# Kernel optimization log

Hardware: AMD Instinct MI355X
Metric: run time of the kernel (lower is better)

The kernel has to match this reference:

```python
import jax, jax.numpy as jnp
import numpy as np

N = 4096          # number of points in the minibatch
POINT_DIM = 64    # latent/data dimensionality used to synthesize valid distance matrices


def _pairwise_dist(x):
    # x: [N, D] -> [N, N] Euclidean distance matrix
    sq = jnp.sum(x * x, axis=1)
    d2 = sq[:, None] + sq[None, :] - 2.0 * (x @ x.T)
    d = jnp.sqrt(jnp.maximum(d2, 0.0))
    return d * (1.0 - jnp.eye(x.shape[0], dtype=x.dtype))  # exact zero diagonal


def _mst_pairs(D):
    """0-dim Vietoris-Rips persistence pairs == edges of the minimum spanning tree.

    Vectorized Prim's algorithm: lax.scan over N-1 steps, O(N) per step.
    Returns int32 [N-1, 2] (parent, child) edge index pairs. Indices are
    non-differentiable (matches the .detach() in the original module).
    """
    D = jax.lax.stop_gradient(D)
    n = D.shape[0]
    INF = jnp.asarray(jnp.inf, D.dtype)
    in_tree = jnp.zeros(n, dtype=bool).at[0].set(True)
    min_dist = D[0].at[0].set(INF)          # best known edge weight from tree to each node
    parent = jnp.zeros(n, dtype=jnp.int32)  # tree endpoint realizing that edge

    def step(carry, _):
        min_dist, parent, in_tree = carry
        masked = jnp.where(in_tree, INF, min_dist)
        j = jnp.argmin(masked).astype(jnp.int32)
        pair = jnp.stack([parent[j], j])
        in_tree = in_tree.at[j].set(True)
        better = (D[j] < min_dist) & (~in_tree)
        parent = jnp.where(better, j, parent)
        min_dist = jnp.where(better, D[j], min_dist)
        return (min_dist, parent, in_tree), pair

    _, pairs = jax.lax.scan(step, (min_dist, parent, in_tree), None, length=n - 1)
    return pairs  # [N-1, 2]


def _sig_error(s1, s2):
    # ((s1 - s2) ** 2).sum() ** 0.5
    diff = s1 - s2
    return jnp.sqrt(jnp.sum(diff * diff))


def _gather(D, pairs):
    return D[pairs[:, 0], pairs[:, 1]]


def setup_inputs() -> dict:
    key = jax.random.key(0)
    k1, k2 = jax.random.split(key)
    x1 = jax.random.normal(k1, (N, POINT_DIM), dtype=jnp.float32)
    x2 = jax.random.normal(k2, (N, POINT_DIM), dtype=jnp.float32)
    return {
        "distances1": _pairwise_dist(x1),
        "distances2": _pairwise_dist(x2),
    }


def reference(distances1, distances2):
    # pairs: 0-dim persistence pairings (MST edges), computed on detached distances
    pairs1 = _mst_pairs(distances1)
    pairs2 = _mst_pairs(distances2)

    # match_edges == 'symmetric'
    sig1 = _gather(distances1, pairs1)
    sig1_2 = _gather(distances2, pairs1)
    sig2 = _gather(distances2, pairs2)
    sig2_1 = _gather(distances1, pairs2)

    distance1_2 = _sig_error(sig1, sig1_2)
    distance2_1 = _sig_error(sig2, sig2_1)
    distance = distance1_2 + distance2_1

    # metrics.matched_pairs: |set(pairs1) ∩ set(pairs2)| (MST edges are unique)
    eq = (pairs1[:, None, :] == pairs2[None, :, :]).all(-1)  # [N-1, N-1]
    matched_pairs = jnp.sum(eq.any(-1)).astype(jnp.float32)

    return distance, distance1_2, distance2_1, matched_pairs
```

## Files before the change

### kernel.cpp

```cpp
#include <hip/hip_runtime.h>
#include <math.h>

#define N 4096
#define ROUNDS 12
#define INFKEY 0xFFFFFFFFFFFFFFFFULL
#define LCAP 48
#define EC (N - 1)
#define M2 (2 * EC)
#define MBLK 32
#define RPB (N / MBLK)
#define RPW (RPB / 16)

typedef unsigned long long u64;
typedef unsigned int u32;
typedef unsigned short u16;

#define WS_PARENT(ws) ((int*)((char*)(ws) + 0))
#define WS_RCNT(ws)   ((int*)((char*)(ws) + 32768))
#define WS_RTHR(ws)   ((float*)((char*)(ws) + 65536))
#define WS_EDGES(ws)  ((int2*)((char*)(ws) + 98304))
#define WS_CAND(ws)   ((u64*)((char*)(ws) + 163840))
#define WS_META(ws)   ((int*)((char*)(ws) + 294912))
#define WS_LISTS(ws)  ((u64*)((char*)(ws) + 295168))


__device__ __forceinline__ void mat_barrier(int* cnt, int* gen, int target) {
    __syncthreads();
    if (threadIdx.x == 0) {
        __threadfence();
        int old = atomicAdd(cnt, 1);
        if (old == MBLK - 1) {
            __hip_atomic_store(cnt, 0, __ATOMIC_RELAXED, __HIP_MEMORY_SCOPE_AGENT);
            __hip_atomic_store(gen, target, __ATOMIC_RELEASE, __HIP_MEMORY_SCOPE_AGENT);
        } else {
            while (__hip_atomic_load(gen, __ATOMIC_ACQUIRE, __HIP_MEMORY_SCOPE_AGENT) < target)
                __builtin_amdgcn_s_sleep(1);
        }
        __threadfence();
    }
    __syncthreads();
}

__global__ __launch_bounds__(1024) void build_kernel(const float* __restrict__ D1,
                                                     const float* __restrict__ D2,
                                                     int* __restrict__ rowcount,
                                                     float* __restrict__ rthresh,
                                                     u64* __restrict__ lists,
                                                     u64* __restrict__ cand,
                                                     int* __restrict__ meta) {
    const int gb = blockIdx.x;
    const int tid = threadIdx.x;

    if (gb < 4) {
        int i = (gb * 1024 + tid) * 4;
        cand[i] = INFKEY; cand[i + 1] = INFKEY; cand[i + 2] = INFKEY; cand[i + 3] = INFKEY;
    } else if (gb == 4 && tid < 64) {
        meta[tid] = 0;
    }

    const int m = gb >> 8;
    const int wid = tid >> 6, lane = tid & 63;
    const int row = (gb & 255) * 16 + wid;
    const float* __restrict__ Drow = (m ? D2 : D1) + (size_t)row * N;
    const float INF = __builtin_inff();

    float4 v[16];
#pragma unroll
    for (int it = 0; it < 16; ++it)
        v[it] = *(const float4*)(Drow + it * 256 + lane * 4);

    float mn = INF, sm = 0.f;
#pragma unroll
    for (int it = 0; it < 16; ++it) {
        float a = v[it].x, b = v[it].y, c = v[it].z, d = v[it].w;
        mn = fminf(mn, a > 0.f ? a : INF);
        mn = fminf(mn, b > 0.f ? b : INF);
        mn = fminf(mn, c > 0.f ? c : INF);
        mn = fminf(mn, d > 0.f ? d : INF);
        sm += a + b + c + d;
    }
#pragma unroll
    for (int off = 32; off > 0; off >>= 1) {
        mn = fminf(mn, __shfl_xor(mn, off, 64));
        sm += __shfl_xor(sm, off, 64);
    }
    const float mean = sm * (1.f / 4095.f);
    float T = mn + 0.25f * (mean - mn);

    int mycnt, total;
    for (int iter = 0; iter < 10; ++iter) {
        mycnt = 0;
#pragma unroll
        for (int it = 0; it < 16; ++it) {
            mycnt += (v[it].x > 0.f && v[it].x < T);
            mycnt += (v[it].y > 0.f && v[it].y < T);
            mycnt += (v[it].z > 0.f && v[it].z < T);
            mycnt += (v[it].w > 0.f && v[it].w < T);
        }
        total = mycnt;
#pragma unroll
        for (int off = 32; off > 0; off >>= 1) total += __shfl_xor(total, off, 64);
        if (total <= LCAP) break;
        T = mn + 0.5f * (T - mn);
    }

    int incl = mycnt;
#pragma unroll
    for (int d = 1; d < 64; d <<= 1) {
        int o = __shfl_up(incl, d, 64);
        if (lane >= d) incl += o;
    }
    int pos = incl - mycnt;

    u64* lp = lists + ((size_t)m * N + row) * LCAP;
#pragma unroll
    for (int it = 0; it < 16; ++it) {
        float e4[4] = {v[it].x, v[it].y, v[it].z, v[it].w};
#pragma unroll
        for (int s = 0; s < 4; ++s) {
            float x = e4[s];
            if (x > 0.f && x < T) {
                if (pos < LCAP)
                    lp[pos] = ((u64)__float_as_uint(x) << 12) | (unsigned)(it * 256 + lane * 4 + s);
                ++pos;
            }
        }
    }
    if (lane == 0) {
        rowcount[m * N + row] = total;
        rthresh[m * N + row] = T;
    }
}

__global__ __launch_bounds__(1024) void solve_kernel(const float* __restrict__ D1,
                                                     const float* __restrict__ D2,
                                                     const int* __restrict__ rcnt,
                                                     const float* __restrict__ rthr,
                                                     const u64* __restrict__ lists,
                                                     u64* __restrict__ cand_g,
                                                     int2* __restrict__ edges_g,
                                                     int* __restrict__ parent_g,
                                                     int* __restrict__ meta,
                                                     float* __restrict__ out) {
    const int b = blockIdx.x;
    const int m = b / MBLK;
    const int bm = b - m * MBLK;
    const int tid = threadIdx.x;
    const int wid = tid >> 6, lane = tid & 63;
    const float* __restrict__ D = m ? D2 : D1;
    const int* __restrict__ grc = rcnt + m * N;
    const float* __restrict__ gth = rthr + m * N;
    const u64* __restrict__ gls = lists + (size_t)m * N * LCAP;
    int2* __restrict__ ged = edges_g + (size_t)m * N;
    int* __restrict__ gpar = parent_g + m * N;
    int* bcnt = meta + m * 16 + 1;
    int* bgen = meta + m * 16 + 2;
    int* garr = meta + 40;
    const float INF = __builtin_inff();

    __shared__ __align__(16) char SM[57344];
    int* scomp = (int*)SM;
    u64* scand = (u64*)(SM + 16384);
    u16* sresc = (u16*)(SM + 49152);
    __shared__ int snres, secnt, scnt, swar[16];

    for (int i = tid; i < N; i += 1024) scomp[i] = i;
    if (tid == 0) secnt = 0;
    int phase = 0;
    bool done = false;

    for (int round = 0; round < ROUNDS && !done; ++round) {
        const int buf = round & 1;
        u64* __restrict__ gcand = cand_g + (size_t)buf * 2 * N + m * N;
        u64* __restrict__ gcand_o = cand_g + (size_t)(buf ^ 1) * 2 * N + m * N;

        for (int i = tid; i < N; i += 1024) scand[i] = INFKEY;
        if (tid == 0) snres = 0;
        __syncthreads();

        for (int r = 0; r < RPW; ++r) {
            const int row = bm * RPB + wid * RPW + r;
            const int c = scomp[row];
            const int cnt = grc[row];
            const bool forced = (cnt > LCAP);
            u64 best = INFKEY;
            if (!forced && lane < cnt) {
                u64 e = gls[(size_t)row * LCAP + lane];
                int j = (int)(e & 0xFFF);
                if (scomp[j] != c) best = e;
            }
#pragma unroll
            for (int off = 32; off > 0; off >>= 1) {
                u64 o = __shfl_xor(best, off, 64);
                if (o < best) best = o;
            }
            if (lane == 0) {
                if (best != INFKEY) {
                    u64 key = ((best >> 12) << 24) | ((u64)row << 12) | (best & 0xFFF);
                    if (key < scand[c]) atomicMin(&scand[c], key);
                } else {
                    int i = atomicAdd(&snres, 1);
                    sresc[i] = (u16)(row | (forced ? 0x4000 : 0x1000));
                }
            }
        }
        __syncthreads();
        for (int c = tid; c < N; c += 1024) {
            u64 v = scand[c];
            if (v != INFKEY) atomicMin(&gcand[c], v);
        }
        mat_barrier(bcnt, bgen, ++phase);

        for (int i = tid + bm * 0; i < RPB; i += 1024)
            if (tid < RPB) gcand_o[bm * RPB + tid] = INFKEY;
        for (int i = tid; i < snres; i += 1024) {
            u16 e = sresc[i];
            if (e & 0x1000) {
                int row = e & 0xFFF;
                int c = scomp[row];
                u64 cc = gcand[c];
                float w = (cc == INFKEY) ? INF : __uint_as_float((u32)(cc >> 24));
                if (!(gth[row] < w)) sresc[i] = 0xFFFF;
            }
        }
        __syncthreads();
        {
            const int nres = snres;
            for (int i = wid; i < nres; i += 16) {
                u16 e = sresc[i];
                if (e == 0xFFFF) continue;
                int row = (int)(e & 0xFFF);
                int c = scomp[row];
                const float* Drow = D + (size_t)row * N;
                u64 best = INFKEY;
                for (int j0 = lane * 4; j0 < N; j0 += 256) {
                    float4 d = *(const float4*)(Drow + j0);
                    int4 cj = *(const int4*)(scomp + j0);
                    if (cj.x != c) { u64 k = ((u64)__float_as_uint(d.x) << 12) | (unsigned)(j0 + 0); if (k < best) best = k; }
                    if (cj.y != c) { u64 k = ((u64)__float_as_uint(d.y) << 12) | (unsigned)(j0 + 1); if (k < best) best = k; }
                    if (cj.z != c) { u64 k = ((u64)__float_as_uint(d.z) << 12) | (unsigned)(j0 + 2); if (k < best) best = k; }
                    if (cj.w != c) { u64 k = ((u64)__float_as_uint(d.w) << 12) | (unsigned)(j0 + 3); if (k < best) best = k; }
                }
#pragma unroll
                for (int off = 32; off > 0; off >>= 1) {
                    u64 o = __shfl_xor(best, off, 64);
                    if (o < best) best = o;
                }
                if (lane == 0 && best != INFKEY) {
                    u64 key = ((best >> 12) << 24) | ((u64)row << 12) | (best & 0xFFF);
                    atomicMin(&gcand[c], key);
                }
            }
        }
        mat_barrier(bcnt, bgen, ++phase);

        for (int i = tid; i < N; i += 1024) scand[i] = gcand[i];
        __syncthreads();
        u16* slink = sresc;
        for (int c = tid; c < N; c += 1024) {
            int l = scomp[c];
            if (l == c) {
                u64 k = scand[c];
                if (k != INFKEY) {
                    int v = (int)(k & 0xFFF);
                    int u = (int)((k >> 12) & 0xFFF);
                    int t = scomp[v];
                    u64 tk = scand[t];
                    int mutual = 0;
                    if (tk != INFKEY) {
                        int tv = (int)(tk & 0xFFF);
                        mutual = (scomp[tv] == c);
                    }
                    if (mutual) {
                        if (c < t) {
                            if (bm == 0) { int idx = atomicAdd(&secnt, 1); ged[idx] = make_int2(u, v); }
                        } else l = t;
                    } else {
                        if (bm == 0) { int idx = atomicAdd(&secnt, 1); ged[idx] = make_int2(u, v); }
                        l = t;
                    }
                }
            }
            slink[c] = (u16)l;
        }
        __syncthreads();
        for (int c = tid; c < N; c += 1024) scomp[c] = slink[c];
        __syncthreads();
        for (int c = tid; c < N; c += 1024) {
            int r = scomp[c];
            int n = scomp[r];
            while (n != r) { r = n; n = scomp[r]; }
            scomp[c] = r;
        }
        __syncthreads();
        if (tid == 0) scnt = 0;
        __syncthreads();
        int local = 0;
        for (int c = tid; c < N; c += 1024) local += (scomp[c] == c) ? 1 : 0;
        atomicAdd(&scnt, local);
        __syncthreads();
        done = (scnt == 1);
        __syncthreads();
    }

    if (bm == 0) {
        u32* uvp  = (u32*)SM;
        u16* off  = (u16*)(SM + 16384);
        u16* adj  = (u16*)(SM + 24576);
        u16* succ = (u16*)(SM + 40960);
        u16* rnk  = (u16*)(SM + 16384);
        u32* minp = (u32*)(SM + 40960);

        __syncthreads();
        const int ec = secnt;
        for (int i = tid; i < ec; i += 1024) {
            int2 e = ged[i];
            uvp[i] = ((u32)e.x << 16) | (u32)e.y;
        }
        for (int i = tid; i < 2048; i += 1024) ((u32*)off)[i] = 0;
        __syncthreads();
        for (int i = tid; i < ec; i += 1024) {
            u32 w = uvp[i];
            int u = (int)(w >> 16), v = (int)(w & 0xFFFF);
            atomicAdd((u32*)off + (u >> 1), 1u << ((u & 1) * 16));
            atomicAdd((u32*)off + (v >> 1), 1u << ((v & 1) * 16));
        }
        __syncthreads();
        {
            const int i0 = tid * 4;
            int d0 = off[i0], d1 = off[i0 + 1], d2 = off[i0 + 2], d3 = off[i0 + 3];
            int t0 = d0, t01 = d0 + d1, t012 = t01 + d2, tot = t012 + d3;
            int inc = tot;
#pragma unroll
            for (int d = 1; d < 64; d <<= 1) {
                int o = __shfl_up(inc, d, 64);
                if (lane >= d) inc += o;
            }
            if (lane == 63) swar[wid] = inc;
            __syncthreads();
            if (wid == 0) {
                int v = (lane < 16) ? swar[lane] : 0;
                int vin = v;
#pragma unroll
                for (int d = 1; d < 16; d <<= 1) {
                    int o = __shfl_up(v, d, 64);
                    if (lane >= d) v += o;
                }
                if (lane < 16) swar[lane] = v - vin;
            }
            __syncthreads();
            int base = swar[wid] + (inc - tot);
            off[i0] = (u16)base;
            off[i0 + 1] = (u16)(base + t0);
            off[i0 + 2] = (u16)(base + t01);
            off[i0 + 3] = (u16)(base + t012);
        }
        __syncthreads();
        for (int e = tid; e < M2; e += 1024) {
            int i = e >> 1;
            u32 w = uvp[i];
            int src = (e & 1) ? (int)(w & 0xFFFF) : (int)(w >> 16);
            u32 old = atomicAdd((u32*)off + (src >> 1), 1u << ((src & 1) * 16));
            u32 slot = (old >> ((src & 1) * 16)) & 0xFFFFu;
            adj[slot] = (u16)e;
            succ[e] = (u16)slot;
        }
        __syncthreads();
        const int e0 = adj[0];
        {
            u16 nsv[8];
            int k = 0;
            for (int e = tid; e < M2; e += 1024) {
                int i = e >> 1;
                u32 w = uvp[i];
                int v = (e & 1) ? (int)(w >> 16) : (int)(w & 0xFFFF);
                int st = succ[e ^ 1];
                int start = (v == 0) ? 0 : off[v - 1];
                int end = off[v];
                int ns = (st + 1 < end) ? st + 1 : start;
                nsv[k++] = adj[ns];
            }
            __syncthreads();
            k = 0;
            for (int e = tid; e < M2; e += 1024) succ[e] = nsv[k++];
        }
        __syncthreads();
        for (int e = tid; e < M2; e += 1024) {
            u16 s = succ[e];
            if (s == (u16)e0) { succ[e] = (u16)e; rnk[e] = 0; }
            else rnk[e] = 1;
        }
        __syncthreads();
        for (int it = 0; it < 13; ++it) {
            u16 nr[8], s2[8];
            int k = 0;
            for (int e = tid; e < M2; e += 1024) {
                u16 s1 = succ[e];
                u16 r1 = rnk[e];
                nr[k] = (u16)(r1 + rnk[s1]);
                s2[k] = succ[s1];
                ++k;
            }
            __syncthreads();
            k = 0;
            for (int e = tid; e < M2; e += 1024) { rnk[e] = nr[k]; succ[e] = s2[k]; ++k; }
            __syncthreads();
        }
        for (int i = tid; i < N; i += 1024) minp[i] = 0xFFFFFFFFu;
        __syncthreads();
        for (int e = tid; e < M2; e += 1024) {
            int i = e >> 1;
            u32 w = uvp[i];
            int dst = (e & 1) ? (int)(w >> 16) : (int)(w & 0xFFFF);
            int srcv = (e & 1) ? (int)(w & 0xFFFF) : (int)(w >> 16);
            u32 p = (u32)(M2 - 1) - (u32)rnk[e];
            atomicMin(&minp[dst], (p << 16) | (u32)srcv);
        }
        __syncthreads();
        for (int v = tid; v < N; v += 1024) gpar[v] = (v == 0) ? 0 : (int)(minp[v] & 0xFFFFu);
    }

    __syncthreads();
    if (tid == 0) {
        __threadfence();
        atomicAdd(garr, 1);
    }
    if (b != 0) return;
    if (tid == 0) {
        while (__hip_atomic_load(garr, __ATOMIC_ACQUIRE, __HIP_MEMORY_SCOPE_AGENT) < 64)
            __builtin_amdgcn_s_sleep(1);
        __threadfence();
    }
    __syncthreads();

    {
        float* rs12 = (float*)SM;
        float* rs21 = (float*)(SM + 64);
        int* rm = (int*)(SM + 128);
        const int* p1 = parent_g;
        const int* p2 = parent_g + N;
        float s12 = 0.f, s21 = 0.f;
        int mcnt = 0;
        for (int c = 1 + tid; c < N; c += 1024) {
            int a = p1[c];
            int bb = p2[c];
            float e1 = D1[(size_t)a * N + c] - D2[(size_t)a * N + c];
            float e2 = D2[(size_t)bb * N + c] - D1[(size_t)bb * N + c];
            s12 += e1 * e1;
            s21 += e2 * e2;
            mcnt += (a == bb) ? 1 : 0;
        }
#pragma unroll
        for (int off = 32; off > 0; off >>= 1) {
            s12 += __shfl_xor(s12, off, 64);
            s21 += __shfl_xor(s21, off, 64);
            mcnt += __shfl_xor(mcnt, off, 64);
        }
        if (lane == 0) { rs12[wid] = s12; rs21[wid] = s21; rm[wid] = mcnt; }
        __syncthreads();
        if (tid == 0) {
            float a = 0.f, bb = 0.f;
            int mm = 0;
#pragma unroll
            for (int w = 0; w < 16; ++w) { a += rs12[w]; bb += rs21[w]; mm += rm[w]; }
            float d12 = sqrtf(a);
            float d21 = sqrtf(bb);
            out[0] = d12 + d21;
            out[1] = d12;
            out[2] = d21;
            out[3] = (float)mm;
        }
    }
}

extern "C" void kernel_launch(void* const* d_in, const int* in_sizes, int n_in,
                              void* d_out, int out_size, void* d_ws, size_t ws_size,
                              hipStream_t stream) {
    const float* D1 = (const float*)d_in[0];
    const float* D2 = (const float*)d_in[1];

    int* parent = WS_PARENT(d_ws);
    int* rcnt = WS_RCNT(d_ws);
    float* rthr = WS_RTHR(d_ws);
    int2* edges = WS_EDGES(d_ws);
    u64* cand = WS_CAND(d_ws);
    int* meta = WS_META(d_ws);
    u64* lists = WS_LISTS(d_ws);

    build_kernel<<<512, 1024, 0, stream>>>(D1, D2, rcnt, rthr, lists, cand, meta);
    solve_kernel<<<2 * MBLK, 1024, 0, stream>>>(D1, D2, rcnt, rthr, lists, cand,
                                                edges, parent, meta, (float*)d_out);
}
```

Measured before the change: 317.5 us.

## Seed first Boruvka round from build kernel and cache exhausted rows

The build kernel now computes each row's nearest neighbour as a packed key and writes it straight into the round-0 candidate buffer. This lets the solve kernel skip the whole candidate-scan phase and its two grid barriers in round 0. Rows whose cached neighbour list has been exhausted are remembered in a shared flag array so later rounds send them directly to the full-row rescan without rereading the list. The list cap is raised from 48 to 64 so fewer rows overflow, and list loads are batched per warp for more memory parallelism, at the cost of more list storage and build-time writes.

After: 309.1 us. 1.03x faster.

```diff
diff --git a/kernel.cpp b/kernel.cpp
--- a/kernel.cpp
+++ b/kernel.cpp
@@ -4,7 +4,7 @@
 #define N 4096
 #define ROUNDS 12
 #define INFKEY 0xFFFFFFFFFFFFFFFFULL
-#define LCAP 48
+#define LCAP 64
 #define EC (N - 1)
 #define M2 (2 * EC)
 #define MBLK 32
@@ -14,6 +14,7 @@
 typedef unsigned long long u64;
 typedef unsigned int u32;
 typedef unsigned short u16;
+typedef unsigned char u8;
 
 #define WS_PARENT(ws) ((int*)((char*)(ws) + 0))
 #define WS_RCNT(ws)   ((int*)((char*)(ws) + 32768))
@@ -51,10 +52,10 @@
     const int gb = blockIdx.x;
     const int tid = threadIdx.x;
 
-    if (gb < 4) {
-        int i = (gb * 1024 + tid) * 4;
+    if (gb < 2) {
+        int i = 2 * N + (gb * 1024 + tid) * 4;
         cand[i] = INFKEY; cand[i + 1] = INFKEY; cand[i + 2] = INFKEY; cand[i + 3] = INFKEY;
-    } else if (gb == 4 && tid < 64) {
+    } else if (gb == 2 && tid < 64) {
         meta[tid] = 0;
     }
 
@@ -69,21 +70,28 @@
     for (int it = 0; it < 16; ++it)
         v[it] = *(const float4*)(Drow + it * 256 + lane * 4);
 
-    float mn = INF, sm = 0.f;
+    u64 kmin = INFKEY;
+    float sm = 0.f;
 #pragma unroll
     for (int it = 0; it < 16; ++it) {
-        float a = v[it].x, b = v[it].y, c = v[it].z, d = v[it].w;
-        mn = fminf(mn, a > 0.f ? a : INF);
-        mn = fminf(mn, b > 0.f ? b : INF);
-        mn = fminf(mn, c > 0.f ? c : INF);
-        mn = fminf(mn, d > 0.f ? d : INF);
-        sm += a + b + c + d;
+        float e4[4] = {v[it].x, v[it].y, v[it].z, v[it].w};
+#pragma unroll
+        for (int s = 0; s < 4; ++s) {
+            float x = e4[s];
+            if (x > 0.f) {
+                u64 k = ((u64)__float_as_uint(x) << 12) | (unsigned)(it * 256 + lane * 4 + s);
+                if (k < kmin) kmin = k;
+            }
+            sm += x;
+        }
     }
 #pragma unroll
     for (int off = 32; off > 0; off >>= 1) {
-        mn = fminf(mn, __shfl_xor(mn, off, 64));
+        u64 o = __shfl_xor(kmin, off, 64);
+        if (o < kmin) kmin = o;
         sm += __shfl_xor(sm, off, 64);
     }
+    const float mn = __uint_as_float((u32)(kmin >> 12));
     const float mean = sm * (1.f / 4095.f);
     float T = mn + 0.25f * (mean - mn);
 
@@ -129,6 +137,7 @@
     if (lane == 0) {
         rowcount[m * N + row] = total;
         rthresh[m * N + row] = T;
+        cand[m * N + row] = ((kmin >> 12) << 24) | ((u64)row << 12) | (kmin & 0xFFF);
     }
 }
 
@@ -162,9 +171,11 @@
     int* scomp = (int*)SM;
     u64* scand = (u64*)(SM + 16384);
     u16* sresc = (u16*)(SM + 49152);
+    __shared__ u8 sexh[RPB];
     __shared__ int snres, secnt, scnt, swar[16];
 
     for (int i = tid; i < N; i += 1024) scomp[i] = i;
+    for (int i = tid; i < RPB; i += 1024) sexh[i] = 0;
     if (tid == 0) secnt = 0;
     int phase = 0;
     bool done = false;
@@ -172,87 +183,110 @@
     for (int round = 0; round < ROUNDS && !done; ++round) {
         const int buf = round & 1;
         u64* __restrict__ gcand = cand_g + (size_t)buf * 2 * N + m * N;
-        u64* __restrict__ gcand_o = cand_g + (size_t)(buf ^ 1) * 2 * N + m * N;
-
-        for (int i = tid; i < N; i += 1024) scand[i] = INFKEY;
-        if (tid == 0) snres = 0;
-        __syncthreads();
-
-        for (int r = 0; r < RPW; ++r) {
-            const int row = bm * RPB + wid * RPW + r;
-            const int c = scomp[row];
-            const int cnt = grc[row];
-            const bool forced = (cnt > LCAP);
-            u64 best = INFKEY;
-            if (!forced && lane < cnt) {
-                u64 e = gls[(size_t)row * LCAP + lane];
-                int j = (int)(e & 0xFFF);
-                if (scomp[j] != c) best = e;
-            }
-#pragma unroll
-            for (int off = 32; off > 0; off >>= 1) {
-                u64 o = __shfl_xor(best, off, 64);
-                if (o < best) best = o;
-            }
-            if (lane == 0) {
-                if (best != INFKEY) {
-                    u64 key = ((best >> 12) << 24) | ((u64)row << 12) | (best & 0xFFF);
-                    if (key < scand[c]) atomicMin(&scand[c], key);
-                } else {
-                    int i = atomicAdd(&snres, 1);
-                    sresc[i] = (u16)(row | (forced ? 0x4000 : 0x1000));
-                }
-            }
-        }
-        __syncthreads();
-        for (int c = tid; c < N; c += 1024) {
-            u64 v = scand[c];
-            if (v != INFKEY) atomicMin(&gcand[c], v);
-        }
-        mat_barrier(bcnt, bgen, ++phase);
-
-        for (int i = tid + bm * 0; i < RPB; i += 1024)
-            if (tid < RPB) gcand_o[bm * RPB + tid] = INFKEY;
-        for (int i = tid; i < snres; i += 1024) {
-            u16 e = sresc[i];
-            if (e & 0x1000) {
-                int row = e & 0xFFF;
-                int c = scomp[row];
-                u64 cc = gcand[c];
-                float w = (cc == INFKEY) ? INF : __uint_as_float((u32)(cc >> 24));
-                if (!(gth[row] < w)) sresc[i] = 0xFFFF;
-            }
-        }
-        __syncthreads();
-        {
-            const int nres = snres;
-            for (int i = wid; i < nres; i += 16) {
+
+        if (round > 0) {
+            u64* __restrict__ gcand_o = cand_g + (size_t)(buf ^ 1) * 2 * N + m * N;
+            for (int i = tid; i < N; i += 1024) scand[i] = INFKEY;
+            if (tid == 0) snres = 0;
+            __syncthreads();
+
+            {
+                const int lbase = wid * RPW;
+                int cnts[RPW];
+                u64 ent[RPW];
+#pragma unroll
+                for (int r = 0; r < RPW; ++r) {
+                    int lrow = lbase + r;
+                    cnts[r] = sexh[lrow] ? -1 : grc[bm * RPB + lrow];
+                }
+#pragma unroll
+                for (int r = 0; r < RPW; ++r) {
+                    int lrow = lbase + r;
+                    ent[r] = (cnts[r] > lane) ? gls[(size_t)(bm * RPB + lrow) * LCAP + lane]
+                                              : INFKEY;
+                }
+#pragma unroll
+                for (int r = 0; r < RPW; ++r) {
+                    const int lrow = lbase + r;
+                    const int row = bm * RPB + lrow;
+                    if (cnts[r] < 0) {
+                        if (lane == 0) { int i = atomicAdd(&snres, 1); sresc[i] = (u16)(row | 0x1000); }
+                        continue;
+                    }
+                    if (cnts[r] > LCAP) {
+                        if (lane == 0) { int i = atomicAdd(&snres, 1); sresc[i] = (u16)(row | 0x4000); }
+                        continue;
+                    }
+                    const int c = scomp[row];
+                    u64 e = ent[r];
+                    u64 best = (e != INFKEY && scomp[(int)(e & 0xFFF)] != c) ? e : INFKEY;
+#pragma unroll
+                    for (int off = 32; off > 0; off >>= 1) {
+                        u64 o = __shfl_xor(best, off, 64);
+                        if (o < best) best = o;
+                    }
+                    if (lane == 0) {
+                        if (best != INFKEY) {
+                            u64 key = ((best >> 12) << 24) | ((u64)row << 12) | (best & 0xFFF);
+                            if (key < scand[c]) atomicMin(&scand[c], key);
+                        } else {
+                            sexh[lrow] = 1;
+                            int i = atomicAdd(&snres, 1); sresc[i] = (u16)(row | 0x1000);
+                        }
+                    }
+                }
+            }
+            __syncthreads();
+            for (int c = tid; c < N; c += 1024) {
+                u64 v = scand[c];
+                if (v != INFKEY) atomicMin(&gcand[c], v);
+            }
+            mat_barrier(bcnt, bgen, ++phase);
+
+            if (tid < RPB)
+                __hip_atomic_store(&gcand_o[bm * RPB + tid], INFKEY,
+                                   __ATOMIC_RELAXED, __HIP_MEMORY_SCOPE_AGENT);
+            for (int i = tid; i < snres; i += 1024) {
                 u16 e = sresc[i];
-                if (e == 0xFFFF) continue;
-                int row = (int)(e & 0xFFF);
-                int c = scomp[row];
-                const float* Drow = D + (size_t)row * N;
-                u64 best = INFKEY;
-                for (int j0 = lane * 4; j0 < N; j0 += 256) {
-                    float4 d = *(const float4*)(Drow + j0);
-                    int4 cj = *(const int4*)(scomp + j0);
-                    if (cj.x != c) { u64 k = ((u64)__float_as_uint(d.x) << 12) | (unsigned)(j0 + 0); if (k < best) best = k; }
-                    if (cj.y != c) { u64 k = ((u64)__float_as_uint(d.y) << 12) | (unsigned)(j0 + 1); if (k < best) best = k; }
-                    if (cj.z != c) { u64 k = ((u64)__float_as_uint(d.z) << 12) | (unsigned)(j0 + 2); if (k < best) best = k; }
-                    if (cj.w != c) { u64 k = ((u64)__float_as_uint(d.w) << 12) | (unsigned)(j0 + 3); if (k < best) best = k; }
-                }
-#pragma unroll
-                for (int off = 32; off > 0; off >>= 1) {
-                    u64 o = __shfl_xor(best, off, 64);
-                    if (o < best) best = o;
-                }
-                if (lane == 0 && best != INFKEY) {
-                    u64 key = ((best >> 12) << 24) | ((u64)row << 12) | (best & 0xFFF);
-                    atomicMin(&gcand[c], key);
-                }
-            }
-        }
-        mat_barrier(bcnt, bgen, ++phase);
+                if (e & 0x1000) {
+                    int row = e & 0xFFF;
+                    int c = scomp[row];
+                    u64 cc = gcand[c];
+                    float w = (cc == INFKEY) ? INF : __uint_as_float((u32)(cc >> 24));
+                    if (!(gth[row] < w)) sresc[i] = 0xFFFF;
+                }
+            }
+            __syncthreads();
+            {
+                const int nres = snres;
+                for (int i = wid; i < nres; i += 16) {
+                    u16 e = sresc[i];
+                    if (e == 0xFFFF) continue;
+                    int row = (int)(e & 0xFFF);
+                    int c = scomp[row];
+                    const float* Drow = D + (size_t)row * N;
+                    u64 best = INFKEY;
+                    for (int j0 = lane * 4; j0 < N; j0 += 256) {
+                        float4 d = *(const float4*)(Drow + j0);
+                        int4 cj = *(const int4*)(scomp + j0);
+                        if (cj.x != c) { u64 k = ((u64)__float_as_uint(d.x) << 12) | (unsigned)(j0 + 0); if (k < best) best = k; }
+                        if (cj.y != c) { u64 k = ((u64)__float_as_uint(d.y) << 12) | (unsigned)(j0 + 1); if (k < best) best = k; }
+                        if (cj.z != c) { u64 k = ((u64)__float_as_uint(d.z) << 12) | (unsigned)(j0 + 2); if (k < best) best = k; }
+                        if (cj.w != c) { u64 k = ((u64)__float_as_uint(d.w) << 12) | (unsigned)(j0 + 3); if (k < best) best = k; }
+                    }
+#pragma unroll
+                    for (int off = 32; off > 0; off >>= 1) {
+                        u64 o = __shfl_xor(best, off, 64);
+                        if (o < best) best = o;
+                    }
+                    if (lane == 0 && best != INFKEY) {
+                        u64 key = ((best >> 12) << 24) | ((u64)row << 12) | (best & 0xFFF);
+                        atomicMin(&gcand[c], key);
+                    }
+                }
+            }
+            mat_barrier(bcnt, bgen, ++phase);
+        }
 
         for (int i = tid; i < N; i += 1024) scand[i] = gcand[i];
         __syncthreads();
@@ -427,7 +461,7 @@
     }
     if (b != 0) return;
     if (tid == 0) {
-        while (__hip_atomic_load(garr, __ATOMIC_ACQUIRE, __HIP_MEMORY_SCOPE_AGENT) < 64)
+        while (__hip_atomic_load(garr, __ATOMIC_ACQUIRE, __HIP_MEMORY_SCOPE_AGENT) < 2 * MBLK)
             __builtin_amdgcn_s_sleep(1);
         __threadfence();
     }
```
